# Kernel tuning notes

Measured on AMD Instinct MI355X. Metric: run time of the kernel, lower is better.

## Reference

```python
import jax, jax.numpy as jnp
import numpy as np


def setup_inputs() -> dict:
    key = jax.random.key(0)
    ks = jax.random.split(key, 12)
    B, N, D_in, D = 64, 512, 512, 512
    inp = {
        "x": jax.random.normal(ks[0], (B, N, D_in), dtype=jnp.float32),
        "adj": jax.random.uniform(ks[1], (B, N, N), dtype=jnp.float32),
        "mask": jnp.ones((B, N, 1), dtype=jnp.float32),
        "W_enc": jax.random.normal(ks[2], (D_in, D), dtype=jnp.float32) * (1.0 / np.sqrt(D_in)),
        "b_enc": jnp.zeros((D,), dtype=jnp.float32),
        "Wz": jax.random.normal(ks[3], (D, D), dtype=jnp.float32) * (1.0 / np.sqrt(D)),
        "Uz": jax.random.normal(ks[4], (D, D), dtype=jnp.float32) * (1.0 / np.sqrt(D)),
        "bz": jnp.zeros((D,), dtype=jnp.float32),
        "Wr": jax.random.normal(ks[5], (D, D), dtype=jnp.float32) * (1.0 / np.sqrt(D)),
        "Ur": jax.random.normal(ks[6], (D, D), dtype=jnp.float32) * (1.0 / np.sqrt(D)),
        "br": jnp.zeros((D,), dtype=jnp.float32),
        "Wh": jax.random.normal(ks[7], (D, D), dtype=jnp.float32) * (1.0 / np.sqrt(D)),
        "Uh": jax.random.normal(ks[8], (D, D), dtype=jnp.float32) * (1.0 / np.sqrt(D)),
        "bh": jnp.zeros((D,), dtype=jnp.float32),
        "ba": jnp.zeros((D,), dtype=jnp.float32),
        "steps": 2,
    }
    return inp


def _gru_step(h, adj, mask, Wz, Uz, bz, Wr, Ur, br, Wh, Uh, bh, ba, act):
    # aggregated neighbor messages: [B,N,D]
    a = jnp.einsum('bnm,bmd->bnd', adj, h) + ba
    z = act(a @ Wz + h @ Uz + bz)          # update gate
    r = act(a @ Wr + h @ Ur + br)          # reset gate
    hc = jnp.tanh(a @ Wh + (r * h) @ Uh + bh)
    hc = hc * mask
    return (1.0 - z) * h + z * hc


def reference(x, adj, mask, W_enc, b_enc, Wz, Uz, bz, Wr, Ur, br, Wh, Uh, bh, ba, steps):
    act = jax.nn.relu
    h = mask * act(x @ W_enc + b_enc)      # [B,N,D]
    for _ in range(steps):
        h = _gru_step(h, adj, mask, Wz, Uz, bz, Wr, Ur, br, Wh, Uh, bh, ba, act)
    return h
```

## Files before the change

kernel.cpp:

```cpp
#include <hip/hip_runtime.h>


#define LD 512
#define NNL ((long)LD * LD)
#define BARRIER do { asm volatile("s_barrier" ::: "memory"); \
                     __builtin_amdgcn_sched_barrier(0); } while (0)

typedef unsigned short u16;
typedef _Float16 f16;
typedef f16 f16x8 __attribute__((ext_vector_type(8)));
typedef float f32x4 __attribute__((ext_vector_type(4)));

__device__ __forceinline__ u16 f2h(float f) { f16 h = (f16)f; return *(u16*)&h; }
__device__ __forceinline__ float h2f(u16 b) { f16 h = *(f16*)&b; return (float)h; }

__device__ __forceinline__ void gload16(const void* g, void* l) {
  __builtin_amdgcn_global_load_lds(
      (const __attribute__((address_space(1))) void*)g,
      (__attribute__((address_space(3))) void*)l, 16, 0, 0);
}

__device__ __forceinline__ void vwaitN(int n) {
  if (n == 4)      asm volatile("s_waitcnt vmcnt(4)" ::: "memory");
  else if (n == 3) asm volatile("s_waitcnt vmcnt(3)" ::: "memory");
  else if (n == 2) asm volatile("s_waitcnt vmcnt(2)" ::: "memory");
  else if (n == 1) asm volatile("s_waitcnt vmcnt(1)" ::: "memory");
  else             asm volatile("s_waitcnt vmcnt(0)" ::: "memory");
}

__global__ void cvt_f16(const float* __restrict__ in, u16* __restrict__ out, int n4) {
  int i = blockIdx.x * blockDim.x + threadIdx.x;
  if (i >= n4) return;
  float4 v = reinterpret_cast<const float4*>(in)[i];
  ushort4 o;
  o.x = f2h(v.x); o.y = f2h(v.y); o.z = f2h(v.z); o.w = f2h(v.w);
  reinterpret_cast<ushort4*>(out)[i] = o;
}

__global__ void cvt2h(const float* __restrict__ in, u16* __restrict__ ohi,
                      u16* __restrict__ olo, int n4) {
  int i = blockIdx.x * blockDim.x + threadIdx.x;
  if (i >= n4) return;
  float4 v = reinterpret_cast<const float4*>(in)[i];
  ushort4 h, l;
  h.x = f2h(v.x); l.x = f2h(v.x - h2f(h.x));
  h.y = f2h(v.y); l.y = f2h(v.y - h2f(h.y));
  h.z = f2h(v.z); l.z = f2h(v.z - h2f(h.z));
  h.w = f2h(v.w); l.w = f2h(v.w - h2f(h.w));
  reinterpret_cast<ushort4*>(ohi)[i] = h;
  reinterpret_cast<ushort4*>(olo)[i] = l;
}

__global__ void wconv1(const float* __restrict__ in, u16* __restrict__ out, float scale) {
  __shared__ float sm[32][33];
  int tx = threadIdx.x & 31, ty = threadIdx.x >> 5;
  int k0 = blockIdx.y * 32, n0 = blockIdx.x * 32;
#pragma unroll
  for (int i = 0; i < 32; i += 8)
    sm[ty + i][tx] = in[(size_t)(k0 + ty + i) * LD + n0 + tx];
  __syncthreads();
#pragma unroll
  for (int i = 0; i < 32; i += 8)
    out[(size_t)(n0 + ty + i) * LD + k0 + tx] = f2h(sm[tx][ty + i] * scale);
}

__global__ void wconv2h(const float* __restrict__ in, u16* __restrict__ ohi,
                        u16* __restrict__ olo, float scale) {
  __shared__ float sm[32][33];
  int tx = threadIdx.x & 31, ty = threadIdx.x >> 5;
  int k0 = blockIdx.y * 32, n0 = blockIdx.x * 32;
#pragma unroll
  for (int i = 0; i < 32; i += 8)
    sm[ty + i][tx] = in[(size_t)(k0 + ty + i) * LD + n0 + tx];
  __syncthreads();
#pragma unroll
  for (int i = 0; i < 32; i += 8) {
    float v = sm[tx][ty + i] * scale;
    u16 hi = f2h(v);
    size_t o = (size_t)(n0 + ty + i) * LD + k0 + tx;
    ohi[o] = hi;
    olo[o] = f2h(v - h2f(hi));
  }
}

__global__ void transp16(const u16* __restrict__ in, u16* __restrict__ out) {
  __shared__ u16 sm[64][65];
  int b = blockIdx.z;
  int n0 = blockIdx.y * 64, d0 = blockIdx.x * 64;
  int lane = threadIdx.x & 63, grp = threadIdx.x >> 6;
  const u16* src = in + ((size_t)b * LD + n0) * LD + d0;
#pragma unroll
  for (int i = grp; i < 64; i += 4)
    sm[i][lane] = src[(size_t)i * LD + lane];
  __syncthreads();
  u16* dst = out + ((size_t)b * LD + d0) * LD + n0;
#pragma unroll
  for (int i = grp; i < 64; i += 4)
    dst[(size_t)i * LD + lane] = sm[lane][i];
}

struct LENC {
  enum { P = 3 };
  static constexpr int AI[3] = {0, 1, 1}, BI[3] = {0, 0, 1};
  static constexpr int SA[3] = {1, 1, 0}, SB[3] = {1, 0, 1};
};
struct LA {
  enum { P = 1 };
  static constexpr int AI[1] = {0}, BI[1] = {0};
  static constexpr int SA[1] = {1}, SB[1] = {1};
};
struct LZ {
  enum { P = 2 };
  static constexpr int AI[2] = {0, 1}, BI[2] = {0, 1};
  static constexpr int SA[2] = {1, 1}, SB[2] = {1, 1};
};
struct LR {
  enum { P = 4 };
  static constexpr int AI[4] = {0, 0, 1, 2}, BI[4] = {0, 1, 1, 2};
  static constexpr int SA[4] = {1, 0, 1, 1}, SB[4] = {1, 1, 0, 1};
};
struct LG1 {
  enum { P = 6 };
  static constexpr int AI[6] = {0, 0, 1, 2, 3, 3}, BI[6] = {0, 1, 1, 2, 2, 3};
  static constexpr int SA[6] = {1, 0, 1, 1, 1, 0}, SB[6] = {1, 1, 0, 1, 0, 1};
};
struct LG2 {
  enum { P = 2 };
  static constexpr int AI[2] = {0, 1}, BI[2] = {0, 1};
  static constexpr int SA[2] = {1, 1}, SB[2] = {1, 1};
};

struct Desc {
  const u16* Aop[4];
  const u16* Bop[4];
  const float* bias1;
  const float* mask;
  const float* hf32;
  const u16* z16;
  float* outf;
  u16* o16;
  u16* o16b;
};

template <int EPI, class PL>
__global__ __launch_bounds__(1024, 4) void gemr(Desc d) {
  constexpr int P = PL::P;
  constexpr int NQ = 16 * P;

  __shared__ __align__(16) u16 Aring[3 * 8192];
  __shared__ __align__(16) u16 Bring[3 * 8192];

  const int t = threadIdx.x;
  const int lane = t & 63;
  const int wid = t >> 6;
  const int wr = wid >> 2, wc = wid & 3;

  const int id = (int)blockIdx.x;
  const int swz = (id & 7) * 32 + (id >> 3);
  const int colb = swz & 1;
  const int rowb = swz >> 1;
  size_t baseA, baseB;
  int rowBase0;
  if (EPI == 1) {
    const size_t bz = (size_t)(rowb >> 1);
    baseA = bz * NNL + (size_t)(rowb & 1) * 256 * LD;
    baseB = bz * NNL + (size_t)colb * 256 * LD;
    rowBase0 = (int)bz * 512 + (rowb & 1) * 256;
  } else {
    baseA = (size_t)rowb * 256 * LD;
    baseB = (size_t)colb * 256 * LD;
    rowBase0 = rowb * 256;
  }

  const int sr = t >> 2;
  const int sg = ((t & 3) ^ ((sr & 3) ^ ((sr >> 2) & 3))) * 8;

  auto stA = [&](const u16* op, int kb, int slot) {
    gload16(op + baseA + (size_t)sr * LD + kb + sg, Aring + slot * 8192 + t * 8);
  };
  auto stB = [&](const u16* op, int kb, int slot) {
    gload16(op + baseB + (size_t)sr * LD + kb + sg, Bring + slot * 8192 + t * 8);
  };

  const int lk = lane >> 4;
  const int RA = wr * 64 + (lane & 15);
  const int RB = wc * 64 + (lane & 15);
  const int aoff = RA * 32 + ((lk ^ ((RA & 3) ^ ((RA >> 2) & 3))) * 8);
  const int boff = RB * 32 + ((lk ^ ((RB & 3) ^ ((RB >> 2) & 3))) * 8);

  f32x4 acc[4][4] = {};

  stA(d.Aop[PL::AI[0]], 0, 0);
  stB(d.Bop[PL::BI[0]], 0, 0);
  {
    constexpr int p1c = 1 % P;
    constexpr int kb1 = (1 / P) * 32;
    if (PL::SA[p1c]) stA(d.Aop[PL::AI[p1c]], kb1, 1);
    if (PL::SB[p1c]) stB(d.Bop[PL::BI[p1c]], kb1, 1);
    vwaitN(PL::SA[p1c] + PL::SB[p1c]);
  }
  BARRIER;

  int rA = 0, rB = 0;
  for (int kk = 0; kk < 16; ++kk) {
#pragma unroll
    for (int p = 0; p < P; ++p) {
      const int q = kk * P + p;
      const int p1 = (p + 1) % P, p2 = (p + 2) % P;
      const int kb2 = (p + 2 < P) ? kk * 32 : (p + 2 < 2 * P) ? (kk + 1) * 32 : (kk + 2) * 32;
      const bool st2 = (q + 2) < NQ;

      f16x8 af[4], bf[4];
      {
        const u16* As_ = Aring + rA * 8192;
        const u16* Bs_ = Bring + rB * 8192;
#pragma unroll
        for (int i = 0; i < 4; ++i) af[i] = *(const f16x8*)&As_[aoff + i * 512];
#pragma unroll
        for (int j = 0; j < 4; ++j) bf[j] = *(const f16x8*)&Bs_[boff + j * 512];
      }
      if (st2) {
        if (PL::SA[p2]) stA(d.Aop[PL::AI[p2]], kb2, (rA + PL::SA[p1] + 1) % 3);
        if (PL::SB[p2]) stB(d.Bop[PL::BI[p2]], kb2, (rB + PL::SB[p1] + 1) % 3);
      }
      __builtin_amdgcn_s_setprio(1);
#pragma unroll
      for (int i = 0; i < 4; ++i)
#pragma unroll
        for (int j = 0; j < 4; ++j)
          acc[i][j] = __builtin_amdgcn_mfma_f32_16x16x32_f16(af[i], bf[j], acc[i][j], 0, 0, 0);
      __builtin_amdgcn_s_setprio(0);
      vwaitN(st2 ? PL::SA[p2] + PL::SB[p2] : 0);
      BARRIER;
      rA = (rA + PL::SA[p1]) % 3;
      rB = (rB + PL::SB[p1]) % 3;
    }
  }

  const float S4 = 0.0625f;
  const float S12 = 2.44140625e-4f;
  const int rowBase = rowBase0 + wr * 64 + (lane >> 4) * 4;
  const int colBase = colb * 256 + wc * 64 + (lane & 15);
#pragma unroll
  for (int i = 0; i < 4; ++i) {
#pragma unroll
    for (int j = 0; j < 4; ++j) {
      const int col = colBase + j * 16;
      const float bv = d.bias1[col];
#pragma unroll
      for (int r = 0; r < 4; ++r) {
        const int row = rowBase + i * 16 + r;
        const size_t idx = (size_t)row * LD + col;
        const float a = acc[i][j][r];
        if (EPI == 0) {
          float v = fmaxf(a + bv, 0.0f) * d.mask[row];
          d.outf[idx] = v;
          d.o16[idx] = f2h(v * S4);
        } else if (EPI == 1) {
          float v = a + bv * S4;
          u16 hi = f2h(v);
          d.o16[idx] = hi;
          d.o16b[idx] = f2h(v - h2f(hi));
        } else if (EPI == 2) {
          float v = fmaxf(a + bv, 0.0f);
          d.o16[idx] = f2h(v * S4);
        } else if (EPI == 3) {
          float v = fmaxf(a + bv, 0.0f) * d.hf32[idx];
          u16 hi = f2h(v * S12);
          d.o16[idx] = hi;
          float rec = h2f(hi) * 4096.0f;
          d.o16b[idx] = f2h((v - rec) * S12);
        } else {
          float hc = tanhf(a + bv) * d.mask[row];
          float z = 16.0f * h2f(d.z16[idx]);
          float h = d.hf32[idx];
          float hn = (1.0f - z) * h + z * hc;
          d.outf[idx] = hn;
          d.o16[idx] = f2h(hn * S4);
        }
      }
    }
  }
}

extern "C" void kernel_launch(void* const* d_in, const int* in_sizes, int n_in,
                              void* d_out, int out_size, void* d_ws, size_t ws_size,
                              hipStream_t stream) {
  const float* x    = (const float*)d_in[0];
  const float* adj  = (const float*)d_in[1];
  const float* mask = (const float*)d_in[2];
  const float* Wenc = (const float*)d_in[3];
  const float* benc = (const float*)d_in[4];
  const float* Wz   = (const float*)d_in[5];
  const float* Uz   = (const float*)d_in[6];
  const float* bz_  = (const float*)d_in[7];
  const float* Wr   = (const float*)d_in[8];
  const float* Ur   = (const float*)d_in[9];
  const float* br_  = (const float*)d_in[10];
  const float* Wh   = (const float*)d_in[11];
  const float* Uh   = (const float*)d_in[12];
  const float* bh_  = (const float*)d_in[13];
  const float* ba_  = (const float*)d_in[14];

  float* hf = (float*)d_out;

  const size_t SZ  = (size_t)64 * 512 * 512 * sizeof(u16);
  const size_t WSZ = (size_t)LD * LD * sizeof(u16);
  const size_t NEED = 7 * SZ + 11 * WSZ;
  if (ws_size < NEED) return;

  char* p = (char*)d_ws;
  u16* adj16 = (u16*)p; p += SZ;
  u16* h16   = (u16*)p; p += SZ;
  u16* a_hi  = (u16*)p; p += SZ;
  u16* a_lo  = (u16*)p; p += SZ;
  u16* zht   = (u16*)p; p += SZ;
  u16* rh_hi = (u16*)p; p += SZ;
  u16* rh_lo = (u16*)p; p += SZ;
  u16* w     = (u16*)p;
  u16* We_h = w + 0 * LD * LD;  u16* We_l = w + 1 * LD * LD;
  u16* Wz1  = w + 2 * LD * LD;
  u16* Uz1  = w + 3 * LD * LD;
  u16* Wr_h = w + 4 * LD * LD;  u16* Wr_l = w + 5 * LD * LD;
  u16* Ur1  = w + 6 * LD * LD;
  u16* Wh_h = w + 7 * LD * LD;  u16* Wh_l = w + 8 * LD * LD;
  u16* Uh_h = w + 9 * LD * LD;  u16* Uh_l = w + 10 * LD * LD;
  u16* x_hi = a_hi;
  u16* x_lo = a_lo;

  const int NELT = 64 * 512 * 512;
  cvt2h<<<NELT / 4 / 256, 256, 0, stream>>>(x, x_hi, x_lo, NELT / 4);
  cvt_f16<<<NELT / 4 / 256, 256, 0, stream>>>(adj, adj16, NELT / 4);

  dim3 wg(16, 16);
  wconv2h<<<wg, 256, 0, stream>>>(Wenc, We_h, We_l, 1.0f);
  wconv1<<<wg, 256, 0, stream>>>(Wz, Wz1, 16.0f);
  wconv1<<<wg, 256, 0, stream>>>(Uz, Uz1, 16.0f);
  wconv2h<<<wg, 256, 0, stream>>>(Wr, Wr_h, Wr_l, 16.0f);
  wconv1<<<wg, 256, 0, stream>>>(Ur, Ur1, 16.0f);
  wconv2h<<<wg, 256, 0, stream>>>(Wh, Wh_h, Wh_l, 16.0f);
  wconv2h<<<wg, 256, 0, stream>>>(Uh, Uh_h, Uh_l, 4096.0f);

  {
    Desc d{};
    d.Aop[0] = x_lo; d.Aop[1] = x_hi;
    d.Bop[0] = We_h; d.Bop[1] = We_l;
    d.bias1 = benc; d.mask = mask; d.outf = hf; d.o16 = h16;
    gemr<0, LENC><<<256, 1024, 0, stream>>>(d);
  }

  for (int s = 0; s < 2; ++s) {
    transp16<<<dim3(8, 8, 64), 256, 0, stream>>>(h16, zht);
    {
      Desc d{};
      d.Aop[0] = adj16; d.Bop[0] = zht;
      d.bias1 = ba_; d.o16 = a_hi; d.o16b = a_lo;
      gemr<1, LA><<<256, 1024, 0, stream>>>(d);
    }
    {
      Desc d{};
      d.Aop[0] = a_hi; d.Aop[1] = h16;
      d.Bop[0] = Wz1;  d.Bop[1] = Uz1;
      d.bias1 = bz_; d.o16 = zht;
      gemr<2, LZ><<<256, 1024, 0, stream>>>(d);
    }
    {
      Desc d{};
      d.Aop[0] = a_hi; d.Aop[1] = a_lo; d.Aop[2] = h16;
      d.Bop[0] = Wr_l; d.Bop[1] = Wr_h; d.Bop[2] = Ur1;
      d.bias1 = br_; d.hf32 = hf; d.o16 = rh_hi; d.o16b = rh_lo;
      gemr<3, LR><<<256, 1024, 0, stream>>>(d);
    }
    if (s == 0) {
      Desc d{};
      d.Aop[0] = a_hi; d.Aop[1] = a_lo; d.Aop[2] = rh_lo; d.Aop[3] = rh_hi;
      d.Bop[0] = Wh_l; d.Bop[1] = Wh_h; d.Bop[2] = Uh_h;  d.Bop[3] = Uh_l;
      d.bias1 = bh_; d.mask = mask; d.hf32 = hf; d.z16 = zht;
      d.outf = hf; d.o16 = h16;
      gemr<4, LG1><<<256, 1024, 0, stream>>>(d);
    } else {
      Desc d{};
      d.Aop[0] = a_hi; d.Aop[1] = rh_hi;
      d.Bop[0] = Wh_h; d.Bop[1] = Uh_h;
      d.bias1 = bh_; d.mask = mask; d.hf32 = hf; d.z16 = zht;
      d.outf = hf; d.o16 = h16;
      gemr<4, LG2><<<256, 1024, 0, stream>>>(d);
    }
  }
}
```

Baseline: 740.0 us.

## Deepen GEMM LDS ring from triple to quad buffering with prefetch distance three

Grows the A and B shared-memory rings from 3 to 4 slots and issues global-to-LDS loads three stages ahead instead of two, adjusting the prologue, slot indexing and vmcnt waits to match. The aim is to hide more global memory latency behind the MFMA work. The cost is LDS use rising from 96KB to 128KB per block, which can lower occupancy, and vmcnt thresholds capped at 4 may over-wait.

```diff
diff --git a/kernel.cpp b/kernel.cpp
--- a/kernel.cpp
+++ b/kernel.cpp
@@ -21,7 +21,7 @@
 }
 
 __device__ __forceinline__ void vwaitN(int n) {
-  if (n == 4)      asm volatile("s_waitcnt vmcnt(4)" ::: "memory");
+  if (n >= 4)      asm volatile("s_waitcnt vmcnt(4)" ::: "memory");
   else if (n == 3) asm volatile("s_waitcnt vmcnt(3)" ::: "memory");
   else if (n == 2) asm volatile("s_waitcnt vmcnt(2)" ::: "memory");
   else if (n == 1) asm volatile("s_waitcnt vmcnt(1)" ::: "memory");
@@ -147,8 +147,8 @@
   constexpr int P = PL::P;
   constexpr int NQ = 16 * P;
 
-  __shared__ __align__(16) u16 Aring[3 * 8192];
-  __shared__ __align__(16) u16 Bring[3 * 8192];
+  __shared__ __align__(16) u16 Aring[4 * 8192];
+  __shared__ __align__(16) u16 Bring[4 * 8192];
 
   const int t = threadIdx.x;
   const int lane = t & 63;
@@ -195,9 +195,15 @@
   {
     constexpr int p1c = 1 % P;
     constexpr int kb1 = (1 / P) * 32;
-    if (PL::SA[p1c]) stA(d.Aop[PL::AI[p1c]], kb1, 1);
-    if (PL::SB[p1c]) stB(d.Bop[PL::BI[p1c]], kb1, 1);
-    vwaitN(PL::SA[p1c] + PL::SB[p1c]);
+    constexpr int sA1 = PL::SA[p1c], sB1 = PL::SB[p1c];
+    if (sA1) stA(d.Aop[PL::AI[p1c]], kb1, sA1);
+    if (sB1) stB(d.Bop[PL::BI[p1c]], kb1, sB1);
+    constexpr int p2c = 2 % P;
+    constexpr int kb2 = (2 / P) * 32;
+    constexpr int sA2 = PL::SA[p2c], sB2 = PL::SB[p2c];
+    if (sA2) stA(d.Aop[PL::AI[p2c]], kb2, sA1 + sA2);
+    if (sB2) stB(d.Bop[PL::BI[p2c]], kb2, sB1 + sB2);
+    vwaitN(sA1 + sB1 + sA2 + sB2);
   }
   BARRIER;
 
@@ -206,9 +212,13 @@
 #pragma unroll
     for (int p = 0; p < P; ++p) {
       const int q = kk * P + p;
-      const int p1 = (p + 1) % P, p2 = (p + 2) % P;
-      const int kb2 = (p + 2 < P) ? kk * 32 : (p + 2 < 2 * P) ? (kk + 1) * 32 : (kk + 2) * 32;
+      const int p1 = (p + 1) % P, p2 = (p + 2) % P, p3 = (p + 3) % P;
+      const int kb3 = (p + 3 < P)     ? kk * 32
+                    : (p + 3 < 2 * P) ? (kk + 1) * 32
+                    : (p + 3 < 3 * P) ? (kk + 2) * 32
+                                      : (kk + 3) * 32;
       const bool st2 = (q + 2) < NQ;
+      const bool st3 = (q + 3) < NQ;
 
       f16x8 af[4], bf[4];
       {
@@ -219,9 +229,13 @@
 #pragma unroll
         for (int j = 0; j < 4; ++j) bf[j] = *(const f16x8*)&Bs_[boff + j * 512];
       }
-      if (st2) {
-        if (PL::SA[p2]) stA(d.Aop[PL::AI[p2]], kb2, (rA + PL::SA[p1] + 1) % 3);
-        if (PL::SB[p2]) stB(d.Bop[PL::BI[p2]], kb2, (rB + PL::SB[p1] + 1) % 3);
+      if (st3) {
+        if (PL::SA[p3])
+          stA(d.Aop[PL::AI[p3]], kb3,
+              (rA + PL::SA[p1] + PL::SA[p2] + PL::SA[p3]) & 3);
+        if (PL::SB[p3])
+          stB(d.Bop[PL::BI[p3]], kb3,
+              (rB + PL::SB[p1] + PL::SB[p2] + PL::SB[p3]) & 3);
       }
       __builtin_amdgcn_s_setprio(1);
 #pragma unroll
@@ -230,10 +244,14 @@
         for (int j = 0; j < 4; ++j)
           acc[i][j] = __builtin_amdgcn_mfma_f32_16x16x32_f16(af[i], bf[j], acc[i][j], 0, 0, 0);
       __builtin_amdgcn_s_setprio(0);
-      vwaitN(st2 ? PL::SA[p2] + PL::SB[p2] : 0);
+      {
+        const int n = (st2 ? PL::SA[p2] + PL::SB[p2] : 0) +
+                      (st3 ? PL::SA[p3] + PL::SB[p3] : 0);
+        vwaitN(n);
+      }
       BARRIER;
-      rA = (rA + PL::SA[p1]) % 3;
-      rB = (rB + PL::SB[p1]) % 3;
+      rA = (rA + PL::SA[p1]) & 3;
+      rB = (rB + PL::SB[p1]) & 3;
     }
   }
 
```

Measured after the change: 747.3 us. About the same (+1.0%).
